# Kernel tuning notes

Measured on AMD Instinct MI355X. Metric: run time of the kernel, lower is better.

Reference implementation:

```python
import jax, jax.numpy as jnp
import numpy as np

N_NODES = 50000
N_EDGES = 800000
VOCAB = 1001  # input_dim + 1
HID = 128
OUT = 40
N_LAYERS = 3


def setup_inputs() -> dict:
    key = jax.random.key(0)
    ks = jax.random.split(key, 10)
    feats = jax.random.randint(ks[0], (N_NODES, 2), 0, VOCAB, dtype=jnp.int32)
    src = jax.random.randint(ks[1], (N_EDGES,), 0, N_NODES, dtype=jnp.int32)
    dst = jax.random.randint(ks[2], (N_EDGES,), 0, N_NODES, dtype=jnp.int32)
    s = 1.0 / np.sqrt(HID)
    key_emb = jax.random.normal(ks[3], (VOCAB, HID), jnp.float32)
    val_emb = jax.random.normal(ks[4], (VOCAB, HID), jnp.float32)
    W1 = jax.random.uniform(ks[5], (N_LAYERS, HID, HID), jnp.float32, -s, s)
    b1 = jnp.zeros((N_LAYERS, HID), jnp.float32)
    W2 = jax.random.uniform(ks[6], (N_LAYERS, HID, HID), jnp.float32, -s, s)
    b2 = jnp.zeros((N_LAYERS, HID), jnp.float32)
    Wc = jax.random.uniform(ks[7], (OUT, HID), jnp.float32, -s, s)
    return {"feats": feats, "src": src, "dst": dst, "key_emb": key_emb,
            "val_emb": val_emb, "W1": W1, "b1": b1, "W2": W2, "b2": b2, "Wc": Wc}


def reference(feats, src, dst, key_emb, val_emb, W1, b1, W2, b2, Wc):
    # embedding sum + ReLU: [N, HID]
    h = jax.nn.relu(key_emb[feats[:, 0]] + val_emb[feats[:, 1]])
    for i in range(N_LAYERS):
        # GIN sum aggregation: scatter-add src features to dst; eps = 0
        agg = jax.ops.segment_sum(h[src], dst, num_segments=N_NODES)
        z = h + agg
        # 2-layer MLP (norm='none'): Linear -> ReLU -> Linear
        z = jax.nn.relu(z @ W1[i].T + b1[i])
        h = z @ W2[i].T + b2[i]
        # dropout p=0 -> identity
    return h @ Wc.T
```

## Files before the change

kernel.cpp:

```cpp
#include <hip/hip_runtime.h>

#define N_NODES 50000
#define N_PAD 50048
#define N_EDGES 800000
#define HID 128
#define NBUCK 98
#define BUCK_CAP 8704
#define LBIN_CAP 48
#define ESC_CHUNK 2048
#define ESC_NCHUNK ((N_EDGES + ESC_CHUNK - 1) / ESC_CHUNK)

typedef unsigned int uint;
typedef __attribute__((ext_vector_type(8))) short short8;
typedef __attribute__((ext_vector_type(4))) float f32x4;

__device__ inline uint f2bf_pair(float x, float y) {
    uint ux = __float_as_uint(x);
    uint uy = __float_as_uint(y);
    ux = (ux + 0x7FFFu + ((ux >> 16) & 1u)) >> 16;
    uy = (uy + 0x7FFFu + ((uy >> 16) & 1u)) >> 16;
    return ux | (uy << 16);
}
__device__ inline float bf_lo(uint v) { return __uint_as_float(v << 16); }
__device__ inline float bf_hi(uint v) { return __uint_as_float(v & 0xFFFF0000u); }

__global__ __launch_bounds__(256) void bin_scatter_kernel(const int* __restrict__ src,
                                                          const int* __restrict__ dst,
                                                          int* __restrict__ gcursor,
                                                          uint* __restrict__ col_tmp) {
    __shared__ uint lbin[NBUCK][LBIN_CAP];
    __shared__ int lcnt[NBUCK], gbase[NBUCK];
    int t = threadIdx.x;
    int base = blockIdx.x * ESC_CHUNK;
    if (t < NBUCK) lcnt[t] = 0;
    __syncthreads();
#pragma unroll
    for (int i = 0; i < ESC_CHUNK / 256; ++i) {
        int e = base + i * 256 + t;
        if (e < N_EDGES) {
            int d = dst[e];
            int b = d >> 9;
            uint val = (uint)src[e] | ((uint)(d & 511) << 16);
            int p = atomicAdd(&lcnt[b], 1);
            if (p < LBIN_CAP) {
                lbin[b][p] = val;
            } else {
                int gp = atomicAdd(&gcursor[b], 1);
                if (gp < BUCK_CAP) col_tmp[(size_t)b * BUCK_CAP + gp] = val;
            }
        }
    }
    __syncthreads();
    if (t < NBUCK) {
        int c = lcnt[t];
        if (c > LBIN_CAP) c = LBIN_CAP;
        gbase[t] = atomicAdd(&gcursor[t], c);
    }
    __syncthreads();
    for (int i = t; i < NBUCK * LBIN_CAP; i += 256) {
        int b = i / LBIN_CAP, slot = i % LBIN_CAP;
        int c = lcnt[b];
        if (c > LBIN_CAP) c = LBIN_CAP;
        if (slot < c) {
            int gp = gbase[b] + slot;
            if (gp < BUCK_CAP) col_tmp[(size_t)b * BUCK_CAP + gp] = lbin[b][slot];
        }
    }
}

__global__ __launch_bounds__(512) void bucket_build_kernel(const int* __restrict__ gcursor,
                                                           uint* __restrict__ col_tmp,
                                                           int* __restrict__ row_start,
                                                           int* __restrict__ counts) {
    __shared__ uint edges[BUCK_CAP];
    __shared__ int cnt[512], pre[512], cur[512], s[512];
    int b = blockIdx.x, t = threadIdx.x;
    int cntE = gcursor[b];
    if (cntE > BUCK_CAP) cntE = BUCK_CAP;
    uint* region = col_tmp + (size_t)b * BUCK_CAP;
    for (int i = t; i < cntE; i += 512) edges[i] = region[i];
    cnt[t] = 0;
    cur[t] = 0;
    __syncthreads();
    for (int i = t; i < cntE; i += 512) atomicAdd(&cnt[edges[i] >> 16], 1);
    __syncthreads();
    int v = cnt[t];
    s[t] = v;
    __syncthreads();
    for (int off = 1; off < 512; off <<= 1) {
        int add = (t >= off) ? s[t - off] : 0;
        __syncthreads();
        s[t] += add;
        __syncthreads();
    }
    pre[t] = s[t] - v;
    __syncthreads();
    for (int i = t; i < cntE; i += 512) {
        uint e = edges[i];
        int dl = e >> 16;
        int p = atomicAdd(&cur[dl], 1);
        region[pre[dl] + p] = e & 0xFFFFu;
    }
    int node = b * 512 + t;
    if (node < N_PAD) {
        row_start[node] = b * BUCK_CAP + pre[t];
        counts[node] = cnt[t];
    }
}

#define EMB_BLOCKS ((N_NODES * 32 + 255) / 256)
__global__ void embed_wconv_kernel(const int* __restrict__ feats,
                                   const float* __restrict__ key_emb,
                                   const float* __restrict__ val_emb, uint* __restrict__ h,
                                   const float* __restrict__ W1, const float* __restrict__ W2,
                                   const float* __restrict__ Wc,
                                   uint* __restrict__ w1b, uint* __restrict__ w2b,
                                   uint* __restrict__ wcb) {
    if (blockIdx.x >= EMB_BLOCKS) {
        int i = (blockIdx.x - EMB_BLOCKS) * 256 + threadIdx.x;
        if (i < 3 * 128 * 64) {
            w1b[i] = f2bf_pair(W1[2 * i], W1[2 * i + 1]);
            w2b[i] = f2bf_pair(W2[2 * i], W2[2 * i + 1]);
        }
        if (i < 48 * 64) {
            int r = i >> 6, q = i & 63;
            wcb[i] = (r < 40) ? f2bf_pair(Wc[r * 128 + 2 * q], Wc[r * 128 + 2 * q + 1]) : 0u;
        }
        return;
    }
    int idx = blockIdx.x * 256 + threadIdx.x;
    if (idx >= N_NODES * 32) return;
    int n = idx >> 5, q = idx & 31;
    int f0 = feats[2 * n], f1 = feats[2 * n + 1];
    float4 a = ((const float4*)key_emb)[f0 * 32 + q];
    float4 b = ((const float4*)val_emb)[f1 * 32 + q];
    float r0 = fmaxf(a.x + b.x, 0.f), r1 = fmaxf(a.y + b.y, 0.f);
    float r2 = fmaxf(a.z + b.z, 0.f), r3 = fmaxf(a.w + b.w, 0.f);
    uint2 o;
    o.x = f2bf_pair(r0, r1);
    o.y = f2bf_pair(r2, r3);
    *(uint2*)&h[(size_t)n * 64 + q * 2] = o;
}

__global__ __launch_bounds__(256) void agg_kernel(const uint* __restrict__ hb,
                                                  uint* __restrict__ zb,
                                                  const int* __restrict__ row_start,
                                                  const int* __restrict__ counts,
                                                  const uint* __restrict__ col) {
    int node = blockIdx.x * 4 + (threadIdx.x >> 6);
    int l = threadIdx.x & 63;
    int g = l >> 4, fl = l & 15;
    const uint4* hp4 = (const uint4*)hb;
    int s = __builtin_amdgcn_readfirstlane(row_start[node]);
    int c = __builtin_amdgcn_readfirstlane(counts[node]);
    float a0 = 0.f, a1 = 0.f, a2 = 0.f, a3 = 0.f, a4 = 0.f, a5 = 0.f, a6 = 0.f, a7 = 0.f;
    int j = 0;
#define ACC_ROW(u)                                                        \
    {                                                                     \
        uint4 v = hp4[(size_t)(u) * 16 + fl];                             \
        a0 += bf_lo(v.x); a1 += bf_hi(v.x); a2 += bf_lo(v.y);             \
        a3 += bf_hi(v.y); a4 += bf_lo(v.z); a5 += bf_hi(v.z);             \
        a6 += bf_lo(v.w); a7 += bf_hi(v.w);                               \
    }
    for (; j + 16 <= c; j += 16) {
        int u0 = (int)col[s + j + g];
        int u1 = (int)col[s + j + 4 + g];
        int u2 = (int)col[s + j + 8 + g];
        int u3 = (int)col[s + j + 12 + g];
        ACC_ROW(u0) ACC_ROW(u1) ACC_ROW(u2) ACC_ROW(u3)
    }
    if (j + 8 <= c) {
        int u0 = (int)col[s + j + g];
        int u1 = (int)col[s + j + 4 + g];
        ACC_ROW(u0) ACC_ROW(u1)
        j += 8;
    }
    if (j + 4 <= c) {
        int u = (int)col[s + j + g];
        ACC_ROW(u)
        j += 4;
    }
    if (g < c - j) {
        int u = (int)col[s + j + g];
        ACC_ROW(u)
    }
#undef ACC_ROW
    a0 += __shfl_xor(a0, 16); a1 += __shfl_xor(a1, 16);
    a2 += __shfl_xor(a2, 16); a3 += __shfl_xor(a3, 16);
    a4 += __shfl_xor(a4, 16); a5 += __shfl_xor(a5, 16);
    a6 += __shfl_xor(a6, 16); a7 += __shfl_xor(a7, 16);
    a0 += __shfl_xor(a0, 32); a1 += __shfl_xor(a1, 32);
    a2 += __shfl_xor(a2, 32); a3 += __shfl_xor(a3, 32);
    a4 += __shfl_xor(a4, 32); a5 += __shfl_xor(a5, 32);
    a6 += __shfl_xor(a6, 32); a7 += __shfl_xor(a7, 32);
    if (g == 0) {
        uint4 hv = hp4[(size_t)node * 16 + fl];
        a0 += bf_lo(hv.x); a1 += bf_hi(hv.x); a2 += bf_lo(hv.y); a3 += bf_hi(hv.y);
        a4 += bf_lo(hv.z); a5 += bf_hi(hv.z); a6 += bf_lo(hv.w); a7 += bf_hi(hv.w);
        uint4 o;
        o.x = f2bf_pair(a0, a1);
        o.y = f2bf_pair(a2, a3);
        o.z = f2bf_pair(a4, a5);
        o.w = f2bf_pair(a6, a7);
        ((uint4*)zb)[(size_t)node * 16 + fl] = o;
    }
}

template <bool LAST>
__global__ __launch_bounds__(256) void mlp_kernel(
    const uint* __restrict__ zb, uint* __restrict__ hout,
    const uint* __restrict__ w1b, const float* __restrict__ b1,
    const uint* __restrict__ w2b, const float* __restrict__ b2,
    const uint* __restrict__ wcb, float* __restrict__ out) {
    __shared__ float z1[64][132];
    int t = threadIdx.x;
    int w = t >> 6, l = t & 63;
    int lm = l & 15, lk = l >> 4;
    int row0 = blockIdx.x * 64;

    f32x4 acc[8];
#pragma unroll
    for (int n = 0; n < 8; ++n) {
        float bv = b1[n * 16 + lm];
        acc[n] = (f32x4){bv, bv, bv, bv};
    }
#pragma unroll
    for (int ks = 0; ks < 4; ++ks) {
        uint4 av = *(const uint4*)(zb + (size_t)(row0 + w * 16 + lm) * 64 + ks * 16 + lk * 4);
        short8 a = *(short8*)&av;
#pragma unroll
        for (int n = 0; n < 8; ++n) {
            uint4 bv4 = *(const uint4*)(w1b + (size_t)(n * 16 + lm) * 64 + ks * 16 + lk * 4);
            short8 b = *(short8*)&bv4;
            acc[n] = __builtin_amdgcn_mfma_f32_16x16x32_bf16(a, b, acc[n], 0, 0, 0);
        }
    }
#pragma unroll
    for (int n = 0; n < 8; ++n)
#pragma unroll
        for (int q = 0; q < 4; ++q)
            z1[w * 16 + lk * 4 + q][n * 16 + lm] = fmaxf(acc[n][q], 0.f);

#pragma unroll
    for (int n = 0; n < 8; ++n) {
        float bv = b2[n * 16 + lm];
        acc[n] = (f32x4){bv, bv, bv, bv};
    }
#pragma unroll
    for (int ks = 0; ks < 4; ++ks) {
        float4 f0 = *(const float4*)&z1[w * 16 + lm][ks * 32 + lk * 8];
        float4 f1 = *(const float4*)&z1[w * 16 + lm][ks * 32 + lk * 8 + 4];
        uint4 ua;
        ua.x = f2bf_pair(f0.x, f0.y);
        ua.y = f2bf_pair(f0.z, f0.w);
        ua.z = f2bf_pair(f1.x, f1.y);
        ua.w = f2bf_pair(f1.z, f1.w);
        short8 a = *(short8*)&ua;
#pragma unroll
        for (int n = 0; n < 8; ++n) {
            uint4 bv4 = *(const uint4*)(w2b + (size_t)(n * 16 + lm) * 64 + ks * 16 + lk * 4);
            short8 b = *(short8*)&bv4;
            acc[n] = __builtin_amdgcn_mfma_f32_16x16x32_bf16(a, b, acc[n], 0, 0, 0);
        }
    }
#pragma unroll
    for (int n = 0; n < 8; ++n)
#pragma unroll
        for (int q = 0; q < 4; ++q)
            z1[w * 16 + lk * 4 + q][n * 16 + lm] = acc[n][q];

    if constexpr (!LAST) {
        __syncthreads();
        for (int i = t; i < 2048; i += 256) {
            int row = i >> 5, j = i & 31;
            float4 v = *(const float4*)&z1[row][j * 4];
            uint2 o;
            o.x = f2bf_pair(v.x, v.y);
            o.y = f2bf_pair(v.z, v.w);
            *(uint2*)&hout[(size_t)(row0 + row) * 64 + j * 2] = o;
        }
    } else {
        f32x4 acc3[3];
#pragma unroll
        for (int n = 0; n < 3; ++n) acc3[n] = (f32x4){0.f, 0.f, 0.f, 0.f};
#pragma unroll
        for (int ks = 0; ks < 4; ++ks) {
            float4 f0 = *(const float4*)&z1[w * 16 + lm][ks * 32 + lk * 8];
            float4 f1 = *(const float4*)&z1[w * 16 + lm][ks * 32 + lk * 8 + 4];
            uint4 ua;
            ua.x = f2bf_pair(f0.x, f0.y);
            ua.y = f2bf_pair(f0.z, f0.w);
            ua.z = f2bf_pair(f1.x, f1.y);
            ua.w = f2bf_pair(f1.z, f1.w);
            short8 a = *(short8*)&ua;
#pragma unroll
            for (int n = 0; n < 3; ++n) {
                uint4 bv4 = *(const uint4*)(wcb + (size_t)(n * 16 + lm) * 64 + ks * 16 + lk * 4);
                short8 b = *(short8*)&bv4;
                acc3[n] = __builtin_amdgcn_mfma_f32_16x16x32_bf16(a, b, acc3[n], 0, 0, 0);
            }
        }
#pragma unroll
        for (int n = 0; n < 3; ++n) {
            int cc = n * 16 + lm;
            if (cc < 40) {
#pragma unroll
                for (int q = 0; q < 4; ++q) {
                    int node = row0 + w * 16 + lk * 4 + q;
                    if (node < N_NODES) out[(size_t)node * 40 + cc] = acc3[n][q];
                }
            }
        }
    }
}

extern "C" void kernel_launch(void* const* d_in, const int* in_sizes, int n_in,
                              void* d_out, int out_size, void* d_ws, size_t ws_size,
                              hipStream_t stream) {
    const int* feats = (const int*)d_in[0];
    const int* src = (const int*)d_in[1];
    const int* dst = (const int*)d_in[2];
    const float* key_emb = (const float*)d_in[3];
    const float* val_emb = (const float*)d_in[4];
    const float* W1 = (const float*)d_in[5];
    const float* b1 = (const float*)d_in[6];
    const float* W2 = (const float*)d_in[7];
    const float* b2 = (const float*)d_in[8];
    const float* Wc = (const float*)d_in[9];
    float* out = (float*)d_out;

    char* ws = (char*)d_ws;
    auto carve = [&](size_t bytes) {
        char* p = ws;
        ws += (bytes + 255) & ~(size_t)255;
        return p;
    };
    uint* h0 = (uint*)carve((size_t)N_PAD * 64 * 4);
    uint* h1 = (uint*)carve((size_t)N_PAD * 64 * 4);
    uint* zb = (uint*)carve((size_t)N_PAD * 64 * 4);
    uint* w1b = (uint*)carve((size_t)3 * 128 * 64 * 4);
    uint* w2b = (uint*)carve((size_t)3 * 128 * 64 * 4);
    uint* wcb = (uint*)carve((size_t)48 * 64 * 4);
    int* row_start = (int*)carve((size_t)N_PAD * 4);
    int* counts = (int*)carve((size_t)N_PAD * 4);
    int* gcursor = (int*)carve(512);
    uint* col_tmp = (uint*)carve((size_t)NBUCK * BUCK_CAP * 4);

    hipMemsetAsync(gcursor, 0, 512, stream);

    bin_scatter_kernel<<<ESC_NCHUNK, 256, 0, stream>>>(src, dst, gcursor, col_tmp);
    embed_wconv_kernel<<<EMB_BLOCKS + 96, 256, 0, stream>>>(feats, key_emb, val_emb, h0,
                                                            W1, W2, Wc, w1b, w2b, wcb);
    bucket_build_kernel<<<NBUCK, 512, 0, stream>>>(gcursor, col_tmp, row_start, counts);

    const int NBLK_MLP = (N_PAD + 63) / 64;
    const int NBLK_AGG = (N_NODES + 3) / 4;

    agg_kernel<<<NBLK_AGG, 256, 0, stream>>>(h0, zb, row_start, counts, col_tmp);
    mlp_kernel<false><<<NBLK_MLP, 256, 0, stream>>>(zb, h1, w1b, b1, w2b, b2, nullptr, nullptr);
    agg_kernel<<<NBLK_AGG, 256, 0, stream>>>(h1, zb, row_start, counts, col_tmp);
    mlp_kernel<false><<<NBLK_MLP, 256, 0, stream>>>(zb, h0, w1b + 128 * 64, b1 + HID,
                                                    w2b + 128 * 64, b2 + HID, nullptr, nullptr);
    agg_kernel<<<NBLK_AGG, 256, 0, stream>>>(h0, zb, row_start, counts, col_tmp);
    mlp_kernel<true><<<NBLK_MLP, 256, 0, stream>>>(zb, nullptr, w1b + 2 * 128 * 64, b1 + 2 * HID,
                                                   w2b + 2 * 128 * 64, b2 + 2 * HID, wcb, out);
}
```

Baseline: 306.4 us.

## Split MLP tile into 32 rows with warps sharing output columns

The MLP kernel now handles 32 rows per block instead of 64. Each pair of waves splits the 128 output columns of a 16-row tile, so each wave holds 4 accumulators instead of 8. This halves shared memory and accumulator registers and doubles the block count, aiming for higher occupancy and better load balance. In exchange it adds block barriers between the two GEMMs, since rows are now shared across waves, and it leaves half the waves idle in the final classifier step.

```diff
diff --git a/kernel.cpp b/kernel.cpp
--- a/kernel.cpp
+++ b/kernel.cpp
@@ -212,44 +212,47 @@
     const uint* __restrict__ w1b, const float* __restrict__ b1,
     const uint* __restrict__ w2b, const float* __restrict__ b2,
     const uint* __restrict__ wcb, float* __restrict__ out) {
-    __shared__ float z1[64][132];
+    __shared__ float z1[32][132];
     int t = threadIdx.x;
     int w = t >> 6, l = t & 63;
     int lm = l & 15, lk = l >> 4;
-    int row0 = blockIdx.x * 64;
-
-    f32x4 acc[8];
-#pragma unroll
-    for (int n = 0; n < 8; ++n) {
-        float bv = b1[n * 16 + lm];
+    int rw = (w >> 1) * 16;
+    int n0 = (w & 1) * 4;
+    int row0 = blockIdx.x * 32;
+
+    f32x4 acc[4];
+#pragma unroll
+    for (int n = 0; n < 4; ++n) {
+        float bv = b1[(n0 + n) * 16 + lm];
         acc[n] = (f32x4){bv, bv, bv, bv};
     }
 #pragma unroll
     for (int ks = 0; ks < 4; ++ks) {
-        uint4 av = *(const uint4*)(zb + (size_t)(row0 + w * 16 + lm) * 64 + ks * 16 + lk * 4);
+        uint4 av = *(const uint4*)(zb + (size_t)(row0 + rw + lm) * 64 + ks * 16 + lk * 4);
         short8 a = *(short8*)&av;
 #pragma unroll
-        for (int n = 0; n < 8; ++n) {
-            uint4 bv4 = *(const uint4*)(w1b + (size_t)(n * 16 + lm) * 64 + ks * 16 + lk * 4);
+        for (int n = 0; n < 4; ++n) {
+            uint4 bv4 = *(const uint4*)(w1b + (size_t)((n0 + n) * 16 + lm) * 64 + ks * 16 + lk * 4);
             short8 b = *(short8*)&bv4;
             acc[n] = __builtin_amdgcn_mfma_f32_16x16x32_bf16(a, b, acc[n], 0, 0, 0);
         }
     }
 #pragma unroll
-    for (int n = 0; n < 8; ++n)
+    for (int n = 0; n < 4; ++n)
 #pragma unroll
         for (int q = 0; q < 4; ++q)
-            z1[w * 16 + lk * 4 + q][n * 16 + lm] = fmaxf(acc[n][q], 0.f);
-
-#pragma unroll
-    for (int n = 0; n < 8; ++n) {
-        float bv = b2[n * 16 + lm];
+            z1[rw + lk * 4 + q][(n0 + n) * 16 + lm] = fmaxf(acc[n][q], 0.f);
+    __syncthreads();
+
+#pragma unroll
+    for (int n = 0; n < 4; ++n) {
+        float bv = b2[(n0 + n) * 16 + lm];
         acc[n] = (f32x4){bv, bv, bv, bv};
     }
 #pragma unroll
     for (int ks = 0; ks < 4; ++ks) {
-        float4 f0 = *(const float4*)&z1[w * 16 + lm][ks * 32 + lk * 8];
-        float4 f1 = *(const float4*)&z1[w * 16 + lm][ks * 32 + lk * 8 + 4];
+        float4 f0 = *(const float4*)&z1[rw + lm][ks * 32 + lk * 8];
+        float4 f1 = *(const float4*)&z1[rw + lm][ks * 32 + lk * 8 + 4];
         uint4 ua;
         ua.x = f2bf_pair(f0.x, f0.y);
         ua.y = f2bf_pair(f0.z, f0.w);
@@ -257,21 +260,22 @@
         ua.w = f2bf_pair(f1.z, f1.w);
         short8 a = *(short8*)&ua;
 #pragma unroll
-        for (int n = 0; n < 8; ++n) {
-            uint4 bv4 = *(const uint4*)(w2b + (size_t)(n * 16 + lm) * 64 + ks * 16 + lk * 4);
+        for (int n = 0; n < 4; ++n) {
+            uint4 bv4 = *(const uint4*)(w2b + (size_t)((n0 + n) * 16 + lm) * 64 + ks * 16 + lk * 4);
             short8 b = *(short8*)&bv4;
             acc[n] = __builtin_amdgcn_mfma_f32_16x16x32_bf16(a, b, acc[n], 0, 0, 0);
         }
     }
-#pragma unroll
-    for (int n = 0; n < 8; ++n)
+    __syncthreads();
+#pragma unroll
+    for (int n = 0; n < 4; ++n)
 #pragma unroll
         for (int q = 0; q < 4; ++q)
-            z1[w * 16 + lk * 4 + q][n * 16 + lm] = acc[n][q];
+            z1[rw + lk * 4 + q][(n0 + n) * 16 + lm] = acc[n][q];
+    __syncthreads();
 
     if constexpr (!LAST) {
-        __syncthreads();
-        for (int i = t; i < 2048; i += 256) {
+        for (int i = t; i < 1024; i += 256) {
             int row = i >> 5, j = i & 31;
             float4 v = *(const float4*)&z1[row][j * 4];
             uint2 o;
@@ -280,34 +284,37 @@
             *(uint2*)&hout[(size_t)(row0 + row) * 64 + j * 2] = o;
         }
     } else {
-        f32x4 acc3[3];
-#pragma unroll
-        for (int n = 0; n < 3; ++n) acc3[n] = (f32x4){0.f, 0.f, 0.f, 0.f};
-#pragma unroll
-        for (int ks = 0; ks < 4; ++ks) {
-            float4 f0 = *(const float4*)&z1[w * 16 + lm][ks * 32 + lk * 8];
-            float4 f1 = *(const float4*)&z1[w * 16 + lm][ks * 32 + lk * 8 + 4];
-            uint4 ua;
-            ua.x = f2bf_pair(f0.x, f0.y);
-            ua.y = f2bf_pair(f0.z, f0.w);
-            ua.z = f2bf_pair(f1.x, f1.y);
-            ua.w = f2bf_pair(f1.z, f1.w);
-            short8 a = *(short8*)&ua;
+        if (w < 2) {
+            int rr = w * 16;
+            f32x4 acc3[3];
+#pragma unroll
+            for (int n = 0; n < 3; ++n) acc3[n] = (f32x4){0.f, 0.f, 0.f, 0.f};
+#pragma unroll
+            for (int ks = 0; ks < 4; ++ks) {
+                float4 f0 = *(const float4*)&z1[rr + lm][ks * 32 + lk * 8];
+                float4 f1 = *(const float4*)&z1[rr + lm][ks * 32 + lk * 8 + 4];
+                uint4 ua;
+                ua.x = f2bf_pair(f0.x, f0.y);
+                ua.y = f2bf_pair(f0.z, f0.w);
+                ua.z = f2bf_pair(f1.x, f1.y);
+                ua.w = f2bf_pair(f1.z, f1.w);
+                short8 a = *(short8*)&ua;
+#pragma unroll
+                for (int n = 0; n < 3; ++n) {
+                    uint4 bv4 = *(const uint4*)(wcb + (size_t)(n * 16 + lm) * 64 + ks * 16 + lk * 4);
+                    short8 b = *(short8*)&bv4;
+                    acc3[n] = __builtin_amdgcn_mfma_f32_16x16x32_bf16(a, b, acc3[n], 0, 0, 0);
+                }
+            }
 #pragma unroll
             for (int n = 0; n < 3; ++n) {
-                uint4 bv4 = *(const uint4*)(wcb + (size_t)(n * 16 + lm) * 64 + ks * 16 + lk * 4);
-                short8 b = *(short8*)&bv4;
-                acc3[n] = __builtin_amdgcn_mfma_f32_16x16x32_bf16(a, b, acc3[n], 0, 0, 0);
-            }
-        }
-#pragma unroll
-        for (int n = 0; n < 3; ++n) {
-            int cc = n * 16 + lm;
-            if (cc < 40) {
-#pragma unroll
-                for (int q = 0; q < 4; ++q) {
-                    int node = row0 + w * 16 + lk * 4 + q;
-                    if (node < N_NODES) out[(size_t)node * 40 + cc] = acc3[n][q];
+                int cc = n * 16 + lm;
+                if (cc < 40) {
+#pragma unroll
+                    for (int q = 0; q < 4; ++q) {
+                        int node = row0 + rr + lk * 4 + q;
+                        if (node < N_NODES) out[(size_t)node * 40 + cc] = acc3[n][q];
+                    }
                 }
             }
         }
@@ -353,7 +360,7 @@
                                                             W1, W2, Wc, w1b, w2b, wcb);
     bucket_build_kernel<<<NBUCK, 512, 0, stream>>>(gcursor, col_tmp, row_start, counts);
 
-    const int NBLK_MLP = (N_PAD + 63) / 64;
+    const int NBLK_MLP = N_PAD / 32;
     const int NBLK_AGG = (N_NODES + 3) / 4;
 
     agg_kernel<<<NBLK_AGG, 256, 0, stream>>>(h0, zb, row_start, counts, col_tmp);
```

Measured after the change: 298.6 us. 1.03x faster.
